# Performance work log

Measured on AMD Instinct MI355X. Metric: run time of the kernel, lower is better.

Reference implementation:

```python
import jax, jax.numpy as jnp
import numpy as np

B, T, C = 2, 2048, 1024
H, D = 16, 64


def setup_inputs() -> dict:
    key = jax.random.key(0)
    k1, k2, k3 = jax.random.split(key, 3)
    x = jax.random.normal(k1, (B, T, C), dtype=jnp.float32)
    w_qkv = jax.random.normal(k2, (C, 3 * H * D), dtype=jnp.float32) * (C ** -0.5)
    w_proj = jax.random.normal(k3, (H * D, C), dtype=jnp.float32) * ((H * D) ** -0.5)
    sink_logit = jnp.zeros((H,), dtype=jnp.float32)
    return {"x": x, "w_qkv": w_qkv, "w_proj": w_proj, "sink_logit": sink_logit}


def reference(x, w_qkv, w_proj, sink_logit):
    b, t, c = x.shape
    qkv = x @ w_qkv                                  # [B,T,3HD]
    q, k, v = jnp.split(qkv, 3, axis=-1)
    # [B,H,T,D]
    q = q.reshape(b, t, H, D).transpose(0, 2, 1, 3)
    k = k.reshape(b, t, H, D).transpose(0, 2, 1, 3)
    v = v.reshape(b, t, H, D).transpose(0, 2, 1, 3)

    scale = 1.0 / jnp.sqrt(jnp.asarray(D, dtype=x.dtype))
    scores = jnp.einsum('bhqd,bhkd->bhqk', q, k) * scale   # [B,H,T,T]
    neg_inf = jnp.finfo(x.dtype).min
    causal = jnp.tril(jnp.ones((t, t), dtype=bool))
    scores = jnp.where(causal[None, None], scores, neg_inf)

    # sink column: per-head learnable logit b (added post-scale, V is zero)
    sink = jnp.broadcast_to(sink_logit.reshape(1, H, 1, 1), (b, H, t, 1)).astype(x.dtype)
    aug = jnp.concatenate([sink, scores], axis=-1)          # [B,H,T,T+1]
    attn = jax.nn.softmax(aug, axis=-1)
    # sink V is zero, so drop the sink column for the value contraction
    y = jnp.einsum('bhqk,bhkd->bhqd', attn[..., 1:], v)     # [B,H,T,D]
    y = y.transpose(0, 2, 1, 3).reshape(b, t, H * D)
    return y @ w_proj
```

## Files before the change

kernel.cpp:

```cpp
#include <hip/hip_runtime.h>
#include <hip/hip_bf16.h>
#include <stdint.h>

#define B_ 2
#define T_ 2048
#define C_ 1024
#define H_ 16
#define D_ 64

typedef __attribute__((ext_vector_type(8))) short short8;
typedef __attribute__((ext_vector_type(4))) float floatx4;

__device__ __forceinline__ float bf2f(uint16_t b) {
    return __uint_as_float(((uint32_t)b) << 16);
}
__device__ __forceinline__ uint16_t f2b(float f) {
    __hip_bfloat16 h = __float2bfloat16(f);
    return *(uint16_t*)&h;
}
__device__ __forceinline__ float exp2v(float x) {
    float r;
    asm("v_exp_f32 %0, %1" : "=v"(r) : "v"(x));
    return r;
}
__device__ __forceinline__ uint32_t cvtpk(float lo, float hi) {
    uint32_t r;
    asm("v_cvt_pk_bf16_f32 %0, %1, %2" : "=v"(r) : "v"(lo), "v"(hi));
    return r;
}
__device__ __forceinline__ void glds16(const uint16_t* g, uint16_t* l) {
    __builtin_amdgcn_global_load_lds(
        (const __attribute__((address_space(1))) uint32_t*)g,
        (__attribute__((address_space(3))) uint32_t*)l, 16, 0, 0);
}

__global__ void prep(const float* __restrict__ x, uint16_t* __restrict__ x_c,
                     const float* __restrict__ w_qkv, uint16_t* __restrict__ wt_qkv,
                     const float* __restrict__ w_proj, uint16_t* __restrict__ wt_proj) {
    __shared__ uint16_t tile[32][33];
    int id = blockIdx.x;
    int tid = threadIdx.x;
    if (id < 4096) {
        int i = (id * 256 + tid) * 4;
        float4 v = *(const float4*)(x + i);
        x_c[i + 0] = f2b(v.x);
        x_c[i + 1] = f2b(v.y);
        x_c[i + 2] = f2b(v.z);
        x_c[i + 3] = f2b(v.w);
        return;
    }
    const float* in;
    uint16_t* out;
    int R, W, bx, by;
    if (id < 7168) {
        int tb = id - 4096;
        in = w_qkv; out = wt_qkv; R = 1024; W = 3072;
        bx = tb % 96; by = tb / 96;
    } else {
        int tb = id - 7168;
        in = w_proj; out = wt_proj; R = 1024; W = 1024;
        bx = tb & 31; by = tb >> 5;
    }
    int tx = tid & 31, ty = tid >> 5;
    int c0 = bx * 32, r0 = by * 32;
    #pragma unroll
    for (int i = 0; i < 32; i += 8)
        tile[ty + i][tx] = f2b(in[(size_t)(r0 + ty + i) * W + (c0 + tx)]);
    __syncthreads();
    #pragma unroll
    for (int i = 0; i < 32; i += 8)
        out[(size_t)(c0 + ty + i) * R + (r0 + tx)] = tile[tx][ty + i];
}

template <bool OUT_F32, int BN>
__global__ __launch_bounds__(256, 3)
void gemm_bt(const uint16_t* __restrict__ A, const uint16_t* __restrict__ Bt,
             void* __restrict__ Cv, int M, int N, int K) {
    constexpr int NJ = BN / 32;
    constexpr int BUFB = BN * 32;
    __shared__ uint16_t As[3][128][32];
    __shared__ uint16_t Bs[3][BN][32];
    int tid = threadIdx.x;
    int w = tid >> 6, lane = tid & 63;
    int quad = lane >> 4, l16 = lane & 15;
    int wr = (w >> 1) * 64, wc = (w & 1) * (BN / 2);

    int nwg = gridDim.x;
    int wg = (blockIdx.x & 7) * (nwg >> 3) + (blockIdx.x >> 3);
    int nby = N / BN;
    int row0 = (wg / nby) * 128;
    int col0 = (wg % nby) * BN;

    int sr = w * 32 + (lane >> 2);
    int gscA = ((lane & 3) ^ ((lane >> 2) & 3)) * 8;
    uint16_t* lA0 = &As[0][sr][(lane & 3) * 8];
    const uint16_t* gA = A + (size_t)(row0 + sr) * K + gscA;
    int srB = (BN == 128) ? sr : (tid >> 2);
    int gscB = ((lane & 3) ^ (srB & 3)) * 8;
    uint16_t* lB0 = &Bs[0][srB][(lane & 3) * 8];
    const uint16_t* gB = Bt + (size_t)(col0 + srB) * K + gscB;

    floatx4 acc[4][NJ];
    #pragma unroll
    for (int i = 0; i < 4; i++)
        #pragma unroll
        for (int j = 0; j < NJ; j++)
            acc[i][j] = (floatx4){0.f, 0.f, 0.f, 0.f};

#define STAGE3_(bs_, t_)                                                    \
    {                                                                       \
        const uint16_t* ga_ = gA + (size_t)(t_) * 32;                       \
        const uint16_t* gb_ = gB + (size_t)(t_) * 32;                       \
        uint16_t* la_ = lA0 + (bs_) * 4096;                                 \
        uint16_t* lb_ = lB0 + (bs_) * BUFB;                                 \
        glds16(ga_, la_);                                                   \
        glds16(ga_ + 16 * K, la_ + 512);                                    \
        glds16(gb_, lb_);                                                   \
        if constexpr (BN == 128) glds16(gb_ + 16 * K, lb_ + 512);           \
    }

    int NT = K >> 5;
    STAGE3_(0, 0);
    STAGE3_(1, 1);
    if constexpr (BN == 128)
        asm volatile("s_waitcnt vmcnt(4)" ::: "memory");
    else
        asm volatile("s_waitcnt vmcnt(3)" ::: "memory");
    __builtin_amdgcn_s_barrier();

    const uint16_t* Ab = &As[0][0][0];
    const uint16_t* Bb = &Bs[0][0][0];
    int s = (quad ^ (l16 & 3)) * 8;
    int bc = 0, bs = 2;
    for (int t = 0; t < NT; ++t) {
        if (t + 2 < NT) STAGE3_(bs, t + 2);
        __builtin_amdgcn_sched_barrier(0);
        const uint16_t* Ac = Ab + bc * 4096;
        const uint16_t* Bc = Bb + bc * BUFB;
        short8 af[4], bfr[NJ];
        #pragma unroll
        for (int i = 0; i < 4; i++)
            af[i] = *(const short8*)&Ac[(wr + i * 16 + l16) * 32 + s];
        #pragma unroll
        for (int j = 0; j < NJ; j++)
            bfr[j] = *(const short8*)&Bc[(wc + j * 16 + l16) * 32 + s];
        #pragma unroll
        for (int i = 0; i < 4; i++)
            #pragma unroll
            for (int j = 0; j < NJ; j++)
                acc[i][j] = __builtin_amdgcn_mfma_f32_16x16x32_bf16(
                    af[i], bfr[j], acc[i][j], 0, 0, 0);
        if (t + 2 < NT) {
            if constexpr (BN == 128)
                asm volatile("s_waitcnt vmcnt(4)" ::: "memory");
            else
                asm volatile("s_waitcnt vmcnt(3)" ::: "memory");
        } else {
            asm volatile("s_waitcnt vmcnt(0)" ::: "memory");
        }
        __builtin_amdgcn_s_barrier();
        bc = (bc == 2) ? 0 : bc + 1;
        bs = (bs == 2) ? 0 : bs + 1;
    }
#undef STAGE3_

    #pragma unroll
    for (int i = 0; i < 4; i++) {
        #pragma unroll
        for (int j = 0; j < NJ; j++) {
            int rbase = row0 + wr + i * 16 + quad * 4;
            int cg = col0 + wc + j * 16 + l16;
            #pragma unroll
            for (int r = 0; r < 4; r++) {
                if (OUT_F32)
                    ((float*)Cv)[(size_t)(rbase + r) * N + cg] = acc[i][j][r];
                else
                    ((uint16_t*)Cv)[(size_t)(rbase + r) * N + cg] = f2b(acc[i][j][r]);
            }
        }
    }
}

__global__ __launch_bounds__(256, 4)
void attn_mfma(const uint16_t* __restrict__ qkv,
               const float* __restrict__ sink,
               uint16_t* __restrict__ y) {
    __shared__ uint16_t Vt[2][64][72];
    __shared__ uint16_t Pl[4][16][72];

    int tid = threadIdx.x;
    int w = tid >> 6, lane = tid & 63;
    int quad = lane >> 4, l16 = lane & 15;

    int id = blockIdx.x;
    int strip = 31 - (id >> 5);
    int bh = id & 31;
    int b = bh >> 4, h = bh & 15;
    int q0 = strip * 64 + w * 16;
    int ktiles = strip + 1;

    const uint16_t* qkv_b = qkv + (size_t)b * T_ * 3072;

    const float QSC = 0.125f * 1.44269504f;
    short8 qf[2];
    {
        int qrow = q0 + l16;
        #pragma unroll
        for (int kd = 0; kd < 2; kd++) {
            uint4 raw = *(const uint4*)(qkv_b + (size_t)qrow * 3072 + h * 64 +
                                        kd * 32 + quad * 8);
            const uint16_t* rp = (const uint16_t*)&raw;
            short8 f;
            #pragma unroll
            for (int j = 0; j < 8; j++)
                f[j] = (short)f2b(bf2f(rp[j]) * QSC);
            qf[kd] = f;
        }
    }

    float m_s = sink[h] * 1.44269504f;
    float l_s = 1.0f;
    floatx4 acc_o[4];
    #pragma unroll
    for (int dt = 0; dt < 4; dt++)
        acc_o[dt] = (floatx4){0.f, 0.f, 0.f, 0.f};

    const uint16_t* kfp = qkv_b + 1024 + h * 64 + (size_t)l16 * 3072 + quad * 8;

    int t2 = tid >> 3;
    int dg = tid & 7;
    const uint16_t* vgp = qkv_b + 2048 + h * 64 + (size_t)(2 * t2) * 3072 + dg * 8;
    int vcw = 2 * (t2 ^ (4 * dg));

    uint4 vr0 = *(const uint4*)(vgp);
    uint4 vr1 = *(const uint4*)(vgp + 3072);
    {
        const uint16_t* a0 = (const uint16_t*)&vr0;
        const uint16_t* a1 = (const uint16_t*)&vr1;
        #pragma unroll
        for (int j = 0; j < 8; j++)
            *(uint32_t*)&Vt[0][dg * 8 + j][vcw] =
                (uint32_t)a0[j] | ((uint32_t)a1[j] << 16);
    }
    if (ktiles > 1) {
        vr0 = *(const uint4*)(vgp + 64 * 3072);
        vr1 = *(const uint4*)(vgp + 64 * 3072 + 3072);
    }
    __syncthreads();

    for (int kt = 0; kt < ktiles; kt++) {
        int cur = kt & 1;
        short8 kf[4][2];
        {
            const uint16_t* kp0 = kfp + (size_t)(kt * 64) * 3072;
            #pragma unroll
            for (int rt = 0; rt < 4; rt++) {
                kf[rt][0] = *(const short8*)(kp0 + (size_t)(rt * 16) * 3072);
                kf[rt][1] = *(const short8*)(kp0 + (size_t)(rt * 16) * 3072 + 32);
            }
        }
        if (kt + 1 < ktiles) {
            const uint16_t* a0 = (const uint16_t*)&vr0;
            const uint16_t* a1 = (const uint16_t*)&vr1;
            #pragma unroll
            for (int j = 0; j < 8; j++)
                *(uint32_t*)&Vt[cur ^ 1][dg * 8 + j][vcw] =
                    (uint32_t)a0[j] | ((uint32_t)a1[j] << 16);
        }
        if (kt + 2 < ktiles) {
            size_t off = (size_t)(kt + 2) * 64 * 3072;
            vr0 = *(const uint4*)(vgp + off);
            vr1 = *(const uint4*)(vgp + off + 3072);
        }
        short8 vf[2][4];
        #pragma unroll
        for (int kb = 0; kb < 2; kb++)
            #pragma unroll
            for (int dt = 0; dt < 4; dt++) {
                int d = dt * 16 + l16;
                int col = 2 * (((kb * 16) + quad * 4) ^ (4 * (d >> 3)));
                vf[kb][dt] = *(const short8*)&Vt[cur][d][col];
            }
        floatx4 acc_s[4];
        #pragma unroll
        for (int rt = 0; rt < 4; rt++)
            acc_s[rt] = (floatx4){0.f, 0.f, 0.f, 0.f};
        #pragma unroll
        for (int rt = 0; rt < 4; rt++) {
            acc_s[rt] = __builtin_amdgcn_mfma_f32_16x16x32_bf16(
                kf[rt][0], qf[0], acc_s[rt], 0, 0, 0);
            acc_s[rt] = __builtin_amdgcn_mfma_f32_16x16x32_bf16(
                kf[rt][1], qf[1], acc_s[rt], 0, 0, 0);
        }
        if (kt == strip) {
            int qg = q0 + l16;
            #pragma unroll
            for (int rt = 0; rt < 4; rt++) {
                int kg = kt * 64 + rt * 16 + quad * 4;
                #pragma unroll
                for (int r = 0; r < 4; r++)
                    if (kg + r > qg) acc_s[rt][r] = -1e30f;
            }
        }
        float mx = -1e30f;
        #pragma unroll
        for (int rt = 0; rt < 4; rt++)
            #pragma unroll
            for (int r = 0; r < 4; r++) mx = fmaxf(mx, acc_s[rt][r]);
        mx = fmaxf(mx, __shfl_xor(mx, 16));
        mx = fmaxf(mx, __shfl_xor(mx, 32));
        float mold = m_s;
        if (!__all(mx <= mold + 8.0f)) {
            float mnew = fmaxf(mold, mx);
            float alpha = exp2v(mold - mnew);
            m_s = mnew;
            l_s *= alpha;
            #pragma unroll
            for (int r = 0; r < 4; r++) {
                float ar = __shfl(alpha, (lane & 48) | (quad * 4 + r));
                #pragma unroll
                for (int dt = 0; dt < 4; dt++) acc_o[dt][r] *= ar;
            }
        }
        float mcur = m_s;
        float psum = 0.f;
        #pragma unroll
        for (int rt = 0; rt < 4; rt++) {
            float p0 = exp2v(acc_s[rt][0] - mcur);
            float p1 = exp2v(acc_s[rt][1] - mcur);
            float p2 = exp2v(acc_s[rt][2] - mcur);
            float p3 = exp2v(acc_s[rt][3] - mcur);
            psum += (p0 + p1) + (p2 + p3);
            uint2 pk;
            pk.x = cvtpk(p0, p1);
            pk.y = cvtpk(p2, p3);
            *(uint2*)&Pl[w][l16][rt * 16 + quad * 4] = pk;
        }
        psum += __shfl_xor(psum, 16);
        psum += __shfl_xor(psum, 32);
        l_s += psum;
        #pragma unroll
        for (int kb = 0; kb < 2; kb++) {
            short8 pf = *(const short8*)&Pl[w][l16][kb * 32 + quad * 8];
            #pragma unroll
            for (int dt = 0; dt < 4; dt++)
                acc_o[dt] = __builtin_amdgcn_mfma_f32_16x16x32_bf16(
                    pf, vf[kb][dt], acc_o[dt], 0, 0, 0);
        }
        __syncthreads();
    }

    #pragma unroll
    for (int r = 0; r < 4; r++) {
        float lr = __shfl(l_s, (lane & 48) | (quad * 4 + r));
        float inv = 1.0f / lr;
        int qg = q0 + quad * 4 + r;
        uint16_t* yp = y + (size_t)(b * T_ + qg) * 1024 + h * 64;
        #pragma unroll
        for (int dt = 0; dt < 4; dt++)
            yp[dt * 16 + l16] = f2b(acc_o[dt][r] * inv);
    }
}

extern "C" void kernel_launch(void* const* d_in, const int* in_sizes, int n_in,
                              void* d_out, int out_size, void* d_ws, size_t ws_size,
                              hipStream_t stream) {
    const float* x      = (const float*)d_in[0];
    const float* w_qkv  = (const float*)d_in[1];
    const float* w_proj = (const float*)d_in[2];
    const float* sink   = (const float*)d_in[3];
    float* out          = (float*)d_out;

    char* ws = (char*)d_ws;
    uint16_t* wt_qkv  = (uint16_t*)ws;
    uint16_t* wt_proj = (uint16_t*)(ws + 6291456);
    uint16_t* x_c     = (uint16_t*)(ws + 8388608);
    uint16_t* qkv     = (uint16_t*)(ws + 16777216);
    uint16_t* yb      = (uint16_t*)(ws + 41943040);

    prep<<<dim3(8192), 256, 0, stream>>>(x, x_c, w_qkv, wt_qkv, w_proj, wt_proj);

    gemm_bt<false, 128><<<dim3(768), 256, 0, stream>>>(
        x_c, wt_qkv, qkv, 4096, 3072, 1024);

    attn_mfma<<<dim3(32 * 32), 256, 0, stream>>>(qkv, sink, yb);

    gemm_bt<true, 64><<<dim3(512), 256, 0, stream>>>(
        yb, wt_proj, out, 4096, 1024, 1024);
}
```

Measured before the change: 219.7 us.

## Rewrite attention with 32x32x16 MFMA, transposed scores, and LDS-staged K tiles

```diff
diff --git a/kernel.cpp b/kernel.cpp
--- a/kernel.cpp
+++ b/kernel.cpp
@@ -10,6 +10,7 @@
 
 typedef __attribute__((ext_vector_type(8))) short short8;
 typedef __attribute__((ext_vector_type(4))) float floatx4;
+typedef __attribute__((ext_vector_type(16))) float floatx16;
 
 __device__ __forceinline__ float bf2f(uint16_t b) {
     return __uint_as_float(((uint32_t)b) << 16);
@@ -181,133 +182,126 @@
     }
 }
 
-__global__ __launch_bounds__(256, 4)
+__global__ __launch_bounds__(128, 2)
 void attn_mfma(const uint16_t* __restrict__ qkv,
                const float* __restrict__ sink,
                uint16_t* __restrict__ y) {
+    __shared__ uint16_t Ks[2][64][72];
     __shared__ uint16_t Vt[2][64][72];
-    __shared__ uint16_t Pl[4][16][72];
 
     int tid = threadIdx.x;
     int w = tid >> 6, lane = tid & 63;
-    int quad = lane >> 4, l16 = lane & 15;
+    int l = lane & 31, hi = lane >> 5;
 
     int id = blockIdx.x;
     int strip = 31 - (id >> 5);
     int bh = id & 31;
     int b = bh >> 4, h = bh & 15;
-    int q0 = strip * 64 + w * 16;
+    int q0w = strip * 64 + w * 32;
     int ktiles = strip + 1;
 
     const uint16_t* qkv_b = qkv + (size_t)b * T_ * 3072;
 
     const float QSC = 0.125f * 1.44269504f;
-    short8 qf[2];
+    short8 qf[4];
     {
-        int qrow = q0 + l16;
-        #pragma unroll
-        for (int kd = 0; kd < 2; kd++) {
-            uint4 raw = *(const uint4*)(qkv_b + (size_t)qrow * 3072 + h * 64 +
-                                        kd * 32 + quad * 8);
+        const uint16_t* qp = qkv_b + (size_t)(q0w + l) * 3072 + h * 64 + hi * 8;
+        #pragma unroll
+        for (int kk = 0; kk < 4; kk++) {
+            uint4 raw = *(const uint4*)(qp + kk * 16);
             const uint16_t* rp = (const uint16_t*)&raw;
             short8 f;
             #pragma unroll
             for (int j = 0; j < 8; j++)
                 f[j] = (short)f2b(bf2f(rp[j]) * QSC);
-            qf[kd] = f;
+            qf[kk] = f;
         }
     }
 
     float m_s = sink[h] * 1.44269504f;
     float l_s = 1.0f;
-    floatx4 acc_o[4];
-    #pragma unroll
-    for (int dt = 0; dt < 4; dt++)
-        acc_o[dt] = (floatx4){0.f, 0.f, 0.f, 0.f};
-
-    const uint16_t* kfp = qkv_b + 1024 + h * 64 + (size_t)l16 * 3072 + quad * 8;
-
-    int t2 = tid >> 3;
+    floatx16 acc_o[2];
+    acc_o[0] = (floatx16)0.0f;
+    acc_o[1] = (floatx16)0.0f;
+
+    int g4 = tid >> 3;
     int dg = tid & 7;
-    const uint16_t* vgp = qkv_b + 2048 + h * 64 + (size_t)(2 * t2) * 3072 + dg * 8;
-    int vcw = 2 * (t2 ^ (4 * dg));
-
-    uint4 vr0 = *(const uint4*)(vgp);
-    uint4 vr1 = *(const uint4*)(vgp + 3072);
-    {
-        const uint16_t* a0 = (const uint16_t*)&vr0;
-        const uint16_t* a1 = (const uint16_t*)&vr1;
-        #pragma unroll
-        for (int j = 0; j < 8; j++)
-            *(uint32_t*)&Vt[0][dg * 8 + j][vcw] =
-                (uint32_t)a0[j] | ((uint32_t)a1[j] << 16);
-    }
+    const uint16_t* gkp = qkv_b + 1024 + h * 64 + (size_t)(4 * g4) * 3072 + dg * 8;
+    const uint16_t* gvp = gkp + 1024;
+    int vcol = 4 * ((g4 ^ (2 * dg)) & 15);
+
+    uint4 kq[4], vq[4];
+
+#define STOREV_(buf_)                                                         \
+    {                                                                         \
+        _Pragma("unroll") for (int j = 0; j < 8; j++) {                       \
+            uint2 pr;                                                         \
+            pr.x = (uint32_t)((const uint16_t*)&vq[0])[j] |                   \
+                   ((uint32_t)((const uint16_t*)&vq[1])[j] << 16);            \
+            pr.y = (uint32_t)((const uint16_t*)&vq[2])[j] |                   \
+                   ((uint32_t)((const uint16_t*)&vq[3])[j] << 16);            \
+            *(uint2*)&Vt[buf_][dg * 8 + j][vcol] = pr;                        \
+        }                                                                     \
+    }
+
+    #pragma unroll
+    for (int i = 0; i < 4; i++) {
+        uint4 kv = *(const uint4*)(gkp + (size_t)i * 3072);
+        *(uint4*)&Ks[0][4 * g4 + i][dg * 8] = kv;
+        vq[i] = *(const uint4*)(gvp + (size_t)i * 3072);
+    }
+    STOREV_(0);
     if (ktiles > 1) {
-        vr0 = *(const uint4*)(vgp + 64 * 3072);
-        vr1 = *(const uint4*)(vgp + 64 * 3072 + 3072);
+        #pragma unroll
+        for (int i = 0; i < 4; i++) {
+            kq[i] = *(const uint4*)(gkp + 64 * 3072 + (size_t)i * 3072);
+            vq[i] = *(const uint4*)(gvp + 64 * 3072 + (size_t)i * 3072);
+        }
     }
     __syncthreads();
 
     for (int kt = 0; kt < ktiles; kt++) {
         int cur = kt & 1;
-        short8 kf[4][2];
-        {
-            const uint16_t* kp0 = kfp + (size_t)(kt * 64) * 3072;
-            #pragma unroll
-            for (int rt = 0; rt < 4; rt++) {
-                kf[rt][0] = *(const short8*)(kp0 + (size_t)(rt * 16) * 3072);
-                kf[rt][1] = *(const short8*)(kp0 + (size_t)(rt * 16) * 3072 + 32);
-            }
-        }
         if (kt + 1 < ktiles) {
-            const uint16_t* a0 = (const uint16_t*)&vr0;
-            const uint16_t* a1 = (const uint16_t*)&vr1;
-            #pragma unroll
-            for (int j = 0; j < 8; j++)
-                *(uint32_t*)&Vt[cur ^ 1][dg * 8 + j][vcw] =
-                    (uint32_t)a0[j] | ((uint32_t)a1[j] << 16);
+            #pragma unroll
+            for (int i = 0; i < 4; i++)
+                *(uint4*)&Ks[cur ^ 1][4 * g4 + i][dg * 8] = kq[i];
+            STOREV_(cur ^ 1);
         }
         if (kt + 2 < ktiles) {
             size_t off = (size_t)(kt + 2) * 64 * 3072;
-            vr0 = *(const uint4*)(vgp + off);
-            vr1 = *(const uint4*)(vgp + off + 3072);
-        }
-        short8 vf[2][4];
-        #pragma unroll
-        for (int kb = 0; kb < 2; kb++)
-            #pragma unroll
-            for (int dt = 0; dt < 4; dt++) {
-                int d = dt * 16 + l16;
-                int col = 2 * (((kb * 16) + quad * 4) ^ (4 * (d >> 3)));
-                vf[kb][dt] = *(const short8*)&Vt[cur][d][col];
-            }
-        floatx4 acc_s[4];
-        #pragma unroll
-        for (int rt = 0; rt < 4; rt++)
-            acc_s[rt] = (floatx4){0.f, 0.f, 0.f, 0.f};
-        #pragma unroll
-        for (int rt = 0; rt < 4; rt++) {
-            acc_s[rt] = __builtin_amdgcn_mfma_f32_16x16x32_bf16(
-                kf[rt][0], qf[0], acc_s[rt], 0, 0, 0);
-            acc_s[rt] = __builtin_amdgcn_mfma_f32_16x16x32_bf16(
-                kf[rt][1], qf[1], acc_s[rt], 0, 0, 0);
+            #pragma unroll
+            for (int i = 0; i < 4; i++) {
+                kq[i] = *(const uint4*)(gkp + off + (size_t)i * 3072);
+                vq[i] = *(const uint4*)(gvp + off + (size_t)i * 3072);
+            }
+        }
+        floatx16 s0 = (floatx16)0.0f, s1 = (floatx16)0.0f;
+        #pragma unroll
+        for (int kk = 0; kk < 4; kk++) {
+            short8 k0 = *(const short8*)&Ks[cur][l][kk * 16 + hi * 8];
+            s0 = __builtin_amdgcn_mfma_f32_32x32x16_bf16(k0, qf[kk], s0, 0, 0, 0);
+        }
+        #pragma unroll
+        for (int kk = 0; kk < 4; kk++) {
+            short8 k1 = *(const short8*)&Ks[cur][32 + l][kk * 16 + hi * 8];
+            s1 = __builtin_amdgcn_mfma_f32_32x32x16_bf16(k1, qf[kk], s1, 0, 0, 0);
         }
         if (kt == strip) {
-            int qg = q0 + l16;
-            #pragma unroll
-            for (int rt = 0; rt < 4; rt++) {
-                int kg = kt * 64 + rt * 16 + quad * 4;
-                #pragma unroll
-                for (int r = 0; r < 4; r++)
-                    if (kg + r > qg) acc_s[rt][r] = -1e30f;
-            }
-        }
-        float mx = -1e30f;
-        #pragma unroll
-        for (int rt = 0; rt < 4; rt++)
-            #pragma unroll
-            for (int r = 0; r < 4; r++) mx = fmaxf(mx, acc_s[rt][r]);
-        mx = fmaxf(mx, __shfl_xor(mx, 16));
+            int qg = q0w + l;
+            int kbase = kt * 64 + 4 * hi;
+            #pragma unroll
+            for (int r = 0; r < 16; r++) {
+                int key0 = kbase + (r & 3) + 8 * (r >> 2);
+                if (key0 > qg) s0[r] = -1e30f;
+                if (key0 + 32 > qg) s1[r] = -1e30f;
+            }
+        }
+        float mx = s0[0];
+        #pragma unroll
+        for (int r = 1; r < 16; r++) mx = fmaxf(mx, s0[r]);
+        #pragma unroll
+        for (int r = 0; r < 16; r++) mx = fmaxf(mx, s1[r]);
         mx = fmaxf(mx, __shfl_xor(mx, 32));
         float mold = m_s;
         if (!__all(mx <= mold + 8.0f)) {
@@ -316,49 +310,67 @@
             m_s = mnew;
             l_s *= alpha;
             #pragma unroll
-            for (int r = 0; r < 4; r++) {
-                float ar = __shfl(alpha, (lane & 48) | (quad * 4 + r));
-                #pragma unroll
-                for (int dt = 0; dt < 4; dt++) acc_o[dt][r] *= ar;
+            for (int r = 0; r < 16; r++) {
+                acc_o[0][r] *= alpha;
+                acc_o[1][r] *= alpha;
             }
         }
         float mcur = m_s;
+        float p0[16], p1[16];
         float psum = 0.f;
         #pragma unroll
-        for (int rt = 0; rt < 4; rt++) {
-            float p0 = exp2v(acc_s[rt][0] - mcur);
-            float p1 = exp2v(acc_s[rt][1] - mcur);
-            float p2 = exp2v(acc_s[rt][2] - mcur);
-            float p3 = exp2v(acc_s[rt][3] - mcur);
-            psum += (p0 + p1) + (p2 + p3);
-            uint2 pk;
-            pk.x = cvtpk(p0, p1);
-            pk.y = cvtpk(p2, p3);
-            *(uint2*)&Pl[w][l16][rt * 16 + quad * 4] = pk;
-        }
-        psum += __shfl_xor(psum, 16);
+        for (int r = 0; r < 16; r++) { p0[r] = exp2v(s0[r] - mcur); psum += p0[r]; }
+        #pragma unroll
+        for (int r = 0; r < 16; r++) { p1[r] = exp2v(s1[r] - mcur); psum += p1[r]; }
         psum += __shfl_xor(psum, 32);
         l_s += psum;
-        #pragma unroll
-        for (int kb = 0; kb < 2; kb++) {
-            short8 pf = *(const short8*)&Pl[w][l16][kb * 32 + quad * 8];
-            #pragma unroll
-            for (int dt = 0; dt < 4; dt++)
-                acc_o[dt] = __builtin_amdgcn_mfma_f32_16x16x32_bf16(
-                    pf, vf[kb][dt], acc_o[dt], 0, 0, 0);
+        short8 pf[4];
+        #pragma unroll
+        for (int c = 0; c < 2; c++) {
+            #pragma unroll
+            for (int half = 0; half < 2; half++) {
+                const float* pp = c ? p1 : p0;
+                uint32_t X = cvtpk(pp[half * 8 + 0], pp[half * 8 + 1]);
+                uint32_t Y = cvtpk(pp[half * 8 + 2], pp[half * 8 + 3]);
+                uint32_t Z = cvtpk(pp[half * 8 + 4], pp[half * 8 + 5]);
+                uint32_t W = cvtpk(pp[half * 8 + 6], pp[half * 8 + 7]);
+                asm volatile("v_permlane32_swap_b32 %0, %1" : "+v"(X), "+v"(Z));
+                asm volatile("v_permlane32_swap_b32 %0, %1" : "+v"(Y), "+v"(W));
+                short8 f;
+                ((uint32_t*)&f)[0] = X;
+                ((uint32_t*)&f)[1] = Y;
+                ((uint32_t*)&f)[2] = Z;
+                ((uint32_t*)&f)[3] = W;
+                pf[c * 2 + half] = f;
+            }
+        }
+        #pragma unroll
+        for (int dt = 0; dt < 2; dt++) {
+            int dd = dt * 32 + l;
+            int cb = 2 * (dd >> 3);
+            #pragma unroll
+            for (int ks = 0; ks < 4; ks++) {
+                int col = 4 * ((ks * 4 + hi * 2) ^ cb);
+                short8 v = *(const short8*)&Vt[cur][dd][col];
+                acc_o[dt] = __builtin_amdgcn_mfma_f32_32x32x16_bf16(
+                    v, pf[ks], acc_o[dt], 0, 0, 0);
+            }
         }
         __syncthreads();
     }
-
-    #pragma unroll
-    for (int r = 0; r < 4; r++) {
-        float lr = __shfl(l_s, (lane & 48) | (quad * 4 + r));
-        float inv = 1.0f / lr;
-        int qg = q0 + quad * 4 + r;
-        uint16_t* yp = y + (size_t)(b * T_ + qg) * 1024 + h * 64;
-        #pragma unroll
-        for (int dt = 0; dt < 4; dt++)
-            yp[dt * 16 + l16] = f2b(acc_o[dt][r] * inv);
+#undef STOREV_
+
+    float inv = 1.0f / l_s;
+    uint16_t* yp = y + (size_t)(b * T_ + q0w + l) * 1024 + h * 64;
+    #pragma unroll
+    for (int dt = 0; dt < 2; dt++) {
+        #pragma unroll
+        for (int rb = 0; rb < 4; rb++) {
+            uint2 st;
+            st.x = cvtpk(acc_o[dt][rb * 4 + 0] * inv, acc_o[dt][rb * 4 + 1] * inv);
+            st.y = cvtpk(acc_o[dt][rb * 4 + 2] * inv, acc_o[dt][rb * 4 + 3] * inv);
+            *(uint2*)(yp + dt * 32 + rb * 8 + hi * 4) = st;
+        }
     }
 }
 
@@ -383,7 +395,7 @@
     gemm_bt<false, 128><<<dim3(768), 256, 0, stream>>>(
         x_c, wt_qkv, qkv, 4096, 3072, 1024);
 
-    attn_mfma<<<dim3(32 * 32), 256, 0, stream>>>(qkv, sink, yb);
+    attn_mfma<<<dim3(32 * 32), 128, 0, stream>>>(qkv, sink, yb);
 
     gemm_bt<true, 64><<<dim3(512), 256, 0, stream>>>(
         yb, wt_proj, out, 4096, 1024, 1024);
```

Result: faster. 195.1 us (-11.2%).
